# Kernel optimization log

Measured on AMD Instinct MI355X. Metric: run time of the kernel, lower is better.

Reference implementation:

```python
import jax, jax.numpy as jnp
import numpy as np

L, B, D, H, M, F = 384, 16, 1024, 16, 64, 4096
HD = D // H
LEFT, RIGHT = 64, 64
STD_SCALE = 0.5
LN_EPS = 1e-5


def layer_norm(x, w, b):
    mu = jnp.mean(x, axis=-1, keepdims=True)
    var = jnp.mean((x - mu) ** 2, axis=-1, keepdims=True)
    return (x - mu) / jnp.sqrt(var + LN_EPS) * w + b


def linear(x, w, b):  # torch nn.Linear: y = x @ W^T + b, w is [out, in]
    return x @ w.T + b


def attention_suppression(aw, scale):
    # aw: [N, Tq, Tk] raw logits (may contain -inf)
    p = jax.nn.softmax(aw, axis=-1)
    nz = p > 0.0  # entries with -inf logits are exactly 0 after softmax
    nzs = jnp.sum(nz.astype(aw.dtype), axis=-1, keepdims=True)
    mean = jnp.sum(p, axis=-1, keepdims=True) / nzs
    dis = jnp.where(nz, (p - mean) ** 2, jnp.zeros_like(p))
    var = jnp.sum(dis, axis=-1, keepdims=True) / (nzs - 1.0)
    thr = mean - scale * jnp.sqrt(var)
    return jnp.where(p < thr, -jnp.inf, aw)


def setup_inputs() -> dict:
    key = jax.random.key(0)
    ks = jax.random.split(key, 24)
    s = 0.02

    def w(k, shape):
        return jax.random.normal(k, shape, dtype=jnp.float32) * s

    return {
        "x": jax.random.normal(ks[0], (L, B, D), dtype=jnp.float32),
        "memory": jax.random.normal(ks[1], (M, B, D), dtype=jnp.float32),
        "q_w": w(ks[2], (D, D)), "q_b": jnp.zeros((D,), jnp.float32),
        "k_w": w(ks[3], (D, D)), "k_b": jnp.zeros((D,), jnp.float32),
        "v_w": w(ks[4], (D, D)), "v_b": jnp.zeros((D,), jnp.float32),
        "out_w": w(ks[5], (D, D)), "out_b": jnp.zeros((D,), jnp.float32),
        "ln1_w": jnp.ones((D,), jnp.float32), "ln1_b": jnp.zeros((D,), jnp.float32),
        "fc1_w": w(ks[6], (F, D)), "fc1_b": jnp.zeros((F,), jnp.float32),
        "fc2_w": w(ks[7], (D, F)), "fc2_b": jnp.zeros((D,), jnp.float32),
        "ln2_w": jnp.ones((D,), jnp.float32), "ln2_b": jnp.zeros((D,), jnp.float32),
    }


def reference(x, memory, q_w, q_b, k_w, k_b, v_w, v_b, out_w, out_b,
              ln1_w, ln1_b, fc1_w, fc1_b, fc2_w, fc2_b, ln2_w, ln2_b):
    residual = x
    xn = layer_norm(x, ln1_w, ln1_b)  # normalize_before
    # summarization query = mean over segment (excluding left/right context)
    summary = jnp.mean(xn[LEFT:L - RIGHT], axis=0, keepdims=True)  # [1,B,D]
    inp = jnp.concatenate([xn, summary], axis=0)  # [L+1, B, D]
    mem_and_inp = jnp.concatenate([memory, inp[:-1]], axis=0)  # [M+L, B, D]

    scaling = HD ** -0.5
    q = linear(inp, q_w, q_b) * scaling
    k = linear(mem_and_inp, k_w, k_b)
    v = linear(mem_and_inp, v_w, v_b)

    def split_heads(t):  # [T,B,D] -> [B*H, T, HD]
        return t.reshape(t.shape[0], B * H, HD).transpose(1, 0, 2)

    q, k, v = split_heads(q), split_heads(k), split_heads(v)
    aw = jnp.einsum('nqd,nkd->nqk', q, k)  # [B*H, L+1, M+L]
    # disable mem-on-mem: summary (last) query must not attend to memory keys
    aw = aw.at[:, -1, :M].set(-jnp.inf)
    aw = attention_suppression(aw, STD_SCALE)
    p = jax.nn.softmax(aw, axis=-1)
    attn = jnp.einsum('nqk,nkd->nqd', p, v)  # [B*H, L+1, HD]
    attn = attn.transpose(1, 0, 2).reshape(L + 1, B, D)
    out_and_mem = linear(attn, out_w, out_b)
    # next_m = out_and_mem[-1:] appended to state (identity squash); output drops it
    out = out_and_mem[:-1]

    x = residual + out
    residual = x
    xn = layer_norm(x, ln2_w, ln2_b)
    h = jax.nn.relu(linear(xn, fc1_w, fc1_b))
    h = linear(h, fc2_w, fc2_b)
    return residual + h
```

## Files before the change

### kernel.cpp

```cpp
#include <hip/hip_runtime.h>

typedef __bf16 bf16x8 __attribute__((ext_vector_type(8)));
typedef float f32x4 __attribute__((ext_vector_type(4)));
typedef unsigned short u16x8 __attribute__((ext_vector_type(8)));

__device__ __forceinline__ unsigned short f2bf(float f) {
  union { float f; unsigned int u; } v; v.f = f;
  unsigned int r = v.u + 0x7fffu + ((v.u >> 16) & 1u);
  return (unsigned short)(r >> 16);
}

__device__ __forceinline__ void async16(const unsigned short* g, unsigned short* l) {
  __builtin_amdgcn_global_load_lds(
      (const __attribute__((address_space(1))) unsigned int*)g,
      (__attribute__((address_space(3))) unsigned int*)l, 16, 0, 0);
}

__global__ void cvt_all(const float* __restrict__ q_w, const float* __restrict__ k_w,
                        const float* __restrict__ v_w, const float* __restrict__ o_w,
                        const float* __restrict__ f1w, const float* __restrict__ f2w,
                        const float* __restrict__ mem,
                        const float* __restrict__ q_b, const float* __restrict__ k_b,
                        const float* __restrict__ v_b,
                        unsigned short* __restrict__ WQ, unsigned short* __restrict__ WK,
                        unsigned short* __restrict__ WV, unsigned short* __restrict__ WO,
                        unsigned short* __restrict__ WF1, unsigned short* __restrict__ WF2,
                        unsigned short* __restrict__ MEMB, float* __restrict__ QKVB) {
  const int bid = blockIdx.x;
  const float* src; unsigned short* dst; float scale = 1.f; int base;
  if (bid < 1024)       { src = q_w; dst = WQ;  scale = 0.125f; base = 0; }
  else if (bid < 2048)  { src = k_w; dst = WK;  base = 1024; }
  else if (bid < 3072)  { src = v_w; dst = WV;  base = 2048; }
  else if (bid < 4096)  { src = o_w; dst = WO;  base = 3072; }
  else if (bid < 8192)  { src = f1w; dst = WF1; base = 4096; }
  else if (bid < 12288) { src = f2w; dst = WF2; base = 8192; }
  else if (bid < 13312) { src = mem; dst = MEMB; base = 12288; }
  else {
    const int i = (bid - 13312) * 256 + threadIdx.x;
    QKVB[i] = (i < 1024) ? q_b[i] * 0.125f : (i < 2048 ? k_b[i - 1024] : v_b[i - 2048]);
    return;
  }
  const int i = (bid - base) * 256 + threadIdx.x;
  float4 v = ((const float4*)src)[i];
  ushort4 o;
  o.x = f2bf(v.x * scale); o.y = f2bf(v.y * scale);
  o.z = f2bf(v.z * scale); o.w = f2bf(v.w * scale);
  ((ushort4*)dst)[i] = o;
}

template <int PREFILL>
__global__ __launch_bounds__(256) void ln_bf16(
    const float* __restrict__ src, unsigned short* __restrict__ dst,
    const float* __restrict__ g, const float* __restrict__ be,
    const float* __restrict__ fbias, float* __restrict__ dout) {
  const int row = blockIdx.x, tid = threadIdx.x;
  const float4 v = ((const float4*)(src + (size_t)row * 1024))[tid];
  if (PREFILL) {
    const float4 fb = ((const float4*)fbias)[tid];
    float4 r;
    r.x = v.x + fb.x; r.y = v.y + fb.y; r.z = v.z + fb.z; r.w = v.w + fb.w;
    ((float4*)(dout + (size_t)row * 1024))[tid] = r;
  }
  float s = v.x + v.y + v.z + v.w;
  float qq = v.x * v.x + v.y * v.y + v.z * v.z + v.w * v.w;
#pragma unroll
  for (int off = 32; off; off >>= 1) { s += __shfl_xor(s, off); qq += __shfl_xor(qq, off); }
  __shared__ float ps[4], pq[4];
  const int w = tid >> 6, lane = tid & 63;
  if (lane == 0) { ps[w] = s; pq[w] = qq; }
  __syncthreads();
  if (tid == 0) { ps[0] = ps[0] + ps[1] + ps[2] + ps[3]; pq[0] = pq[0] + pq[1] + pq[2] + pq[3]; }
  __syncthreads();
  const float mu = ps[0] * (1.f / 1024.f);
  const float var = pq[0] * (1.f / 1024.f) - mu * mu;
  const float rs = rsqrtf(var + 1e-5f);
  const float4 gv = ((const float4*)g)[tid];
  const float4 bv = ((const float4*)be)[tid];
  ushort4 o;
  o.x = f2bf((v.x - mu) * rs * gv.x + bv.x);
  o.y = f2bf((v.y - mu) * rs * gv.y + bv.y);
  o.z = f2bf((v.z - mu) * rs * gv.z + bv.z);
  o.w = f2bf((v.w - mu) * rs * gv.w + bv.w);
  ((ushort4*)(dst + (size_t)row * 1024))[tid] = o;
}

#define KOFF 6291456ull
#define VOFF 13631488ull
template <int EPI>
__global__ __launch_bounds__(256) void gemm_bt(
    const unsigned short* __restrict__ A, const unsigned short* __restrict__ Bw,
    const float* __restrict__ bias, const float* __restrict__ resid,
    void* __restrict__ Cout, int M, int N, int K, int lda, int ldb, int NBN, int WM) {
  __shared__ __align__(16) unsigned short lA[128 * 32];
  __shared__ __align__(16) unsigned short lB[128 * 32];
  const int tid = threadIdx.x;
  const int w = tid >> 6, lane = tid & 63;
  const int lr = lane & 15, lq = lane >> 4;
  const int l = blockIdx.x;
  const int xcd = l & 7, r = l >> 3;
  const int bm = xcd * WM + (r % WM);
  const int rest = r / WM;
  const int bn = rest % NBN;
  const size_t koff = (size_t)(rest / NBN) * K;
  const unsigned short* Ab = A + (size_t)bm * 128 * lda + koff;
  const unsigned short* Bb = Bw + (size_t)bn * 128 * ldb + koff;
  const int wm = (w & 1) << 6, wn = (w >> 1) << 6;
  f32x4 acc[4][4] = {};
  const int kiters = K >> 5;
  const int c0 = tid, c1 = 256 + tid;
  const int r0 = c0 >> 2, o0 = (c0 & 3) << 3;
  const int r1 = c1 >> 2, o1 = (c1 & 3) << 3;
  for (int kt = 0; kt < kiters; ++kt) {
    const int kb = kt << 5;
    __syncthreads();
    async16(Ab + (size_t)r0 * lda + kb + o0, lA + c0 * 8);
    async16(Bb + (size_t)r0 * ldb + kb + o0, lB + c0 * 8);
    async16(Ab + (size_t)r1 * lda + kb + o1, lA + c1 * 8);
    async16(Bb + (size_t)r1 * ldb + kb + o1, lB + c1 * 8);
    __syncthreads();
    bf16x8 af[4], bfr[4];
#pragma unroll
    for (int i = 0; i < 4; ++i) af[i] = *(const bf16x8*)(lA + (wm + i * 16 + lr) * 32 + lq * 8);
#pragma unroll
    for (int i = 0; i < 4; ++i) bfr[i] = *(const bf16x8*)(lB + (wn + i * 16 + lr) * 32 + lq * 8);
#pragma unroll
    for (int i = 0; i < 4; ++i)
#pragma unroll
      for (int j = 0; j < 4; ++j)
        acc[i][j] = __builtin_amdgcn_mfma_f32_16x16x32_bf16(af[i], bfr[j], acc[i][j], 0, 0, 0);
  }
  const int which = (bn * 128) >> 10;
#pragma unroll
  for (int i = 0; i < 4; ++i) {
#pragma unroll
    for (int j = 0; j < 4; ++j) {
      const int colg = bn * 128 + wn + j * 16 + lr;
      const float bi = (EPI == 6) ? 0.f : bias[colg];
      const int rowg0 = bm * 128 + wm + i * 16 + lq * 4;
#pragma unroll
      for (int r2 = 0; r2 < 4; ++r2) {
        const int rowg = rowg0 + r2;
        const float val = acc[i][j][r2] + bi;
        if (EPI == 5) {
          const int t = rowg >> 4, bb = rowg & 15;
          const int hh = (colg >> 6) & 15, dd = colg & 63;
          const size_t nn = (size_t)(bb * 16 + hh);
          unsigned short* q16 = (unsigned short*)Cout;
          if (which == 0) {
            if (rowg >= 1024) q16[(nn * 384 + (t - 64)) * 64 + dd] = f2bf(val);
          } else if (which == 1) {
            q16[KOFF + (nn * 448 + t) * 64 + dd] = f2bf(val);
          } else {
            q16[VOFF + (nn * 448 + t) * 64 + dd] = f2bf(val);
          }
        } else {
          const size_t idx = (size_t)rowg * N + colg;
          if (EPI == 2) ((float*)Cout)[idx] = val + resid[idx];
          else if (EPI == 3) ((unsigned short*)Cout)[idx] = f2bf(fmaxf(val, 0.f));
          else if (EPI == 6) atomicAdd(&((float*)Cout)[idx], acc[i][j][r2]);
        }
      }
    }
  }
}

#define WAITV10() asm volatile("s_waitcnt vmcnt(10)" ::: "memory")
#define WAITV8()  asm volatile("s_waitcnt vmcnt(8)" ::: "memory")
#define WAITV0()  asm volatile("s_waitcnt vmcnt(0)" ::: "memory")
#define WAITL0()  asm volatile("s_waitcnt lgkmcnt(0)" ::: "memory")
#define BAR()     do { __builtin_amdgcn_s_barrier(); __builtin_amdgcn_sched_barrier(0); } while (0)
#define SCHED()   __builtin_amdgcn_sched_barrier(0)

#define STG_A(bufv, ksv, ktv) do { \
    unsigned short* d_ = (unsigned short*)lA8 + (bufv) * 16384 + (ksv) * 8192; \
    const unsigned short* s_ = Ab + (((ktv) << 6) + ((ksv) << 5)); \
    async16(s_ + (size_t)sr0 * lda + sc0, d_ + ci0 * 8); \
    async16(s_ + (size_t)sr1 * lda + sc1, d_ + ci1 * 8); } while (0)
#define STG_B(bufv, ksv, ktv) do { \
    unsigned short* d_ = (unsigned short*)lB8 + (bufv) * 16384 + (ksv) * 8192; \
    const unsigned short* s_ = Bb + (((ktv) << 6) + ((ksv) << 5)); \
    async16(s_ + (size_t)sr0 * ldb + sc0, d_ + ci0 * 8); \
    async16(s_ + (size_t)sr1 * ldb + sc1, d_ + ci1 * 8); } while (0)
#define RD_A4(dst, bufv, ksv, mh) \
  _Pragma("unroll") \
  for (int i = 0; i < 4; ++i) \
    dst[i] = *(const bf16x8*)((unsigned short*)lA8 + (bufv) * 16384 + (ksv) * 8192 + \
                              (wm * 128 + (mh) * 64 + i * 16 + lr) * 32 + lq * 8)
#define RD_B4(dst, bufv, ksv) \
  _Pragma("unroll") \
  for (int j = 0; j < 4; ++j) \
    dst[j] = *(const bf16x8*)((unsigned short*)lB8 + (bufv) * 16384 + (ksv) * 8192 + \
                              (wn * 64 + j * 16 + lr) * 32 + lq * 8)
#define MFMA16(accbase, av, bv) \
  _Pragma("unroll") \
  for (int i = 0; i < 4; ++i) \
  _Pragma("unroll") \
  for (int j = 0; j < 4; ++j) \
    acc[(accbase) + i][j] = \
        __builtin_amdgcn_mfma_f32_16x16x32_bf16(av[i], bv[j], acc[(accbase) + i][j], 0, 0, 0)

__global__ __launch_bounds__(512, 2) void gemm8_relu(
    const unsigned short* __restrict__ A, const unsigned short* __restrict__ Bw,
    const float* __restrict__ bias, unsigned short* __restrict__ Cout,
    int N, int lda, int ldb, int MT) {
  __shared__ __align__(16) unsigned short lA8[32768];
  __shared__ __align__(16) unsigned short lB8[32768];
  const int tid = threadIdx.x;
  const int w = tid >> 6, lane = tid & 63;
  const int wm = w >> 2, wn = w & 3;
  const int lr = lane & 15, lq = lane >> 4;
  const int bid = blockIdx.x;
  const int xcd = bid & 7, r = bid >> 3;
  const int bm = xcd * MT + (r % MT);
  const int bn = r / MT;
  const unsigned short* Ab = A + (size_t)bm * 256 * lda;
  const unsigned short* Bb = Bw + (size_t)bn * 256 * ldb;
  const int ci0 = tid, ci1 = tid + 512;
  const int sr0 = ci0 >> 2, sc0 = (ci0 & 3) << 3;
  const int sr1 = ci1 >> 2, sc1 = (ci1 & 3) << 3;

  f32x4 acc[8][4] = {};
  bf16x8 aP[4], aN[4], b0[4], b1[4];

  STG_B(0, 0, 0); STG_A(0, 0, 0); STG_B(0, 1, 0); STG_A(0, 1, 0);
  STG_B(1, 0, 1); STG_A(1, 0, 1); STG_B(1, 1, 1); STG_A(1, 1, 1);
  WAITV8();
  BAR();
  RD_A4(aP, 0, 0, 0);
  RD_B4(b0, 0, 0);

  for (int kt = 0; kt < 16; ++kt) {
    const int buf = kt & 1, nbuf = buf ^ 1, kt2 = kt + 2;
    const bool st = kt2 < 16, tail = kt >= 14;
    WAITL0(); if (tail) { WAITV0(); } else { WAITV10(); } BAR();
    if (st) STG_B(buf, 0, kt2);
    RD_A4(aN, buf, 0, 1);
    SCHED();
    __builtin_amdgcn_s_setprio(1);
    MFMA16(0, aP, b0);
    __builtin_amdgcn_s_setprio(0);
    WAITL0(); if (tail) { WAITV0(); } else { WAITV10(); } BAR();
    if (st) STG_A(buf, 0, kt2);
    RD_A4(aP, buf, 1, 0);
    RD_B4(b1, buf, 1);
    SCHED();
    __builtin_amdgcn_s_setprio(1);
    MFMA16(4, aN, b0);
    __builtin_amdgcn_s_setprio(0);
    WAITL0(); if (tail) { WAITV0(); } else { WAITV10(); } BAR();
    if (st) STG_B(buf, 1, kt2);
    RD_A4(aN, buf, 1, 1);
    SCHED();
    __builtin_amdgcn_s_setprio(1);
    MFMA16(0, aP, b1);
    __builtin_amdgcn_s_setprio(0);
    WAITL0(); if (tail) { WAITV0(); } else { WAITV10(); } BAR();
    if (st) STG_A(buf, 1, kt2);
    if (kt < 15) { RD_A4(aP, nbuf, 0, 0); RD_B4(b0, nbuf, 0); }
    SCHED();
    __builtin_amdgcn_s_setprio(1);
    MFMA16(4, aN, b1);
    __builtin_amdgcn_s_setprio(0);
  }

#pragma unroll
  for (int j = 0; j < 4; ++j) {
    const int colg = bn * 256 + wn * 64 + j * 16 + lr;
    const float bi = bias[colg];
#pragma unroll
    for (int i = 0; i < 8; ++i) {
      const int rowg0 = bm * 256 + wm * 128 + i * 16 + lq * 4;
#pragma unroll
      for (int r2 = 0; r2 < 4; ++r2) {
        const float v = acc[i][j][r2] + bi;
        Cout[(size_t)(rowg0 + r2) * N + colg] = f2bf(fmaxf(v, 0.f));
      }
    }
  }
}

__global__ __launch_bounds__(256) void vtrans(const unsigned short* __restrict__ vb,
                                              unsigned short* __restrict__ vt) {
  __shared__ __align__(16) unsigned short ls[64][80];
  const int kc = blockIdx.x, n = blockIdx.y;
  const int tid = threadIdx.x;
#pragma unroll
  for (int i = 0; i < 2; ++i) {
    const int c = i * 256 + tid;
    const int kk = c >> 3, dc = (c & 7) << 3;
    u16x8 val = *(const u16x8*)(vb + ((size_t)n * 448 + kc * 64 + kk) * 64 + dc);
    *(u16x8*)&ls[kk][dc] = val;
  }
  __syncthreads();
#pragma unroll
  for (int i = 0; i < 2; ++i) {
    const int c = i * 256 + tid;
    const int d = c >> 3, kx = (c & 7) << 3;
    u16x8 o;
#pragma unroll
    for (int j = 0; j < 8; ++j) o[j] = ls[kx + j][d];
    *(u16x8*)(vt + ((size_t)n * 64 + d) * 448 + kc * 64 + kx) = o;
  }
}

#define PST 468
__global__ __launch_bounds__(256) void attn_kernel(
    const unsigned short* __restrict__ qt_, const unsigned short* __restrict__ kt_,
    const unsigned short* __restrict__ vt_, unsigned short* __restrict__ attn) {
  __shared__ __align__(16) unsigned short P[16 * PST];
  __shared__ float Rm[4][16], Rs[4][16], Rc[4][16], Rv[4][16], R2[4][16];
  __shared__ __align__(16) float OT[4][16][17];
  const int id = blockIdx.x;
  const int xcd = id & 7, j0 = id >> 3;
  const int n = xcd * 32 + (j0 & 31), qt = j0 >> 5;
  const int b = n >> 4, h = n & 15;
  const int tid = threadIdx.x, w = tid >> 6, lane = tid & 63;
  const int lr = lane & 15, lq = lane >> 4;

  const unsigned short* qp = qt_ + ((size_t)n * 384 + qt * 16 + lr) * 64 + lq * 8;
  const bf16x8 q0 = *(const bf16x8*)qp;
  const bf16x8 q1 = *(const bf16x8*)(qp + 32);

  f32x4 acc[7];
#pragma unroll
  for (int t = 0; t < 7; ++t) {
    const unsigned short* kp = kt_ + ((size_t)n * 448 + (w * 7 + t) * 16 + lr) * 64 + lq * 8;
    const bf16x8 k0 = *(const bf16x8*)kp;
    const bf16x8 k1 = *(const bf16x8*)(kp + 32);
    f32x4 a = {0.f, 0.f, 0.f, 0.f};
    a = __builtin_amdgcn_mfma_f32_16x16x32_bf16(k0, q0, a, 0, 0, 0);
    a = __builtin_amdgcn_mfma_f32_16x16x32_bf16(k1, q1, a, 0, 0, 0);
    acc[t] = a;
  }

  f32x4 m4 = acc[0];
#pragma unroll
  for (int t = 1; t < 7; ++t) {
    m4[0] = fmaxf(m4[0], acc[t][0]); m4[1] = fmaxf(m4[1], acc[t][1]);
    m4[2] = fmaxf(m4[2], acc[t][2]); m4[3] = fmaxf(m4[3], acc[t][3]);
  }
  float m = fmaxf(fmaxf(m4[0], m4[1]), fmaxf(m4[2], m4[3]));
  m = fmaxf(m, __shfl_xor(m, 16));
  m = fmaxf(m, __shfl_xor(m, 32));
  if (lq == 0) Rm[w][lr] = m;
  __syncthreads();
  m = fmaxf(fmaxf(Rm[0][lr], Rm[1][lr]), fmaxf(Rm[2][lr], Rm[3][lr]));

  f32x4 s4 = {0.f, 0.f, 0.f, 0.f}, c4 = {0.f, 0.f, 0.f, 0.f};
#pragma unroll
  for (int t = 0; t < 7; ++t) {
#pragma unroll
    for (int r = 0; r < 4; ++r) {
      const float e = __expf(acc[t][r] - m);
      acc[t][r] = e;
      s4[r] += e;
      if (e > 0.f) c4[r] += 1.f;
    }
  }
  float s = (s4[0] + s4[1]) + (s4[2] + s4[3]);
  float cnt = (c4[0] + c4[1]) + (c4[2] + c4[3]);
  s += __shfl_xor(s, 16); s += __shfl_xor(s, 32);
  cnt += __shfl_xor(cnt, 16); cnt += __shfl_xor(cnt, 32);
  if (lq == 0) { Rs[w][lr] = s; Rc[w][lr] = cnt; }
  __syncthreads();
  s = (Rs[0][lr] + Rs[1][lr]) + (Rs[2][lr] + Rs[3][lr]);
  cnt = (Rc[0][lr] + Rc[1][lr]) + (Rc[2][lr] + Rc[3][lr]);
  const float inv = 1.f / s;
  const float mean = 1.f / cnt;

  f32x4 d4 = {0.f, 0.f, 0.f, 0.f};
#pragma unroll
  for (int t = 0; t < 7; ++t) {
#pragma unroll
    for (int r = 0; r < 4; ++r) {
      const float p = acc[t][r] * inv;
      const float dd = p - mean;
      if (acc[t][r] > 0.f) d4[r] += dd * dd;
    }
  }
  float dv = (d4[0] + d4[1]) + (d4[2] + d4[3]);
  dv += __shfl_xor(dv, 16); dv += __shfl_xor(dv, 32);
  if (lq == 0) Rv[w][lr] = dv;
  __syncthreads();
  dv = (Rv[0][lr] + Rv[1][lr]) + (Rv[2][lr] + Rv[3][lr]);
  const float thr = mean - 0.5f * sqrtf(dv / (cnt - 1.f));

  f32x4 t4 = {0.f, 0.f, 0.f, 0.f};
#pragma unroll
  for (int t = 0; t < 7; ++t) {
#pragma unroll
    for (int r = 0; r < 4; ++r) {
      if (!(acc[t][r] * inv < thr)) t4[r] += acc[t][r];
    }
  }
  float s2 = (t4[0] + t4[1]) + (t4[2] + t4[3]);
  s2 += __shfl_xor(s2, 16); s2 += __shfl_xor(s2, 32);
  if (lq == 0) R2[w][lr] = s2;
  __syncthreads();
  s2 = (R2[0][lr] + R2[1][lr]) + (R2[2][lr] + R2[3][lr]);
  const float inv2 = 1.f / s2;

#pragma unroll
  for (int t = 0; t < 7; ++t) {
#pragma unroll
    for (int rp = 0; rp < 4; rp += 2) {
      const float v0 = (acc[t][rp] * inv < thr) ? 0.f : acc[t][rp] * inv2;
      const float v1 = (acc[t][rp + 1] * inv < thr) ? 0.f : acc[t][rp + 1] * inv2;
      const unsigned int u = (unsigned int)f2bf(v0) | ((unsigned int)f2bf(v1) << 16);
      *(unsigned int*)&P[lr * PST + (w * 7 + t) * 16 + lq * 4 + rp] = u;
    }
  }
  __syncthreads();

  f32x4 o = {0.f, 0.f, 0.f, 0.f};
#pragma unroll
  for (int c = 0; c < 14; ++c) {
    union { ushort4 hh[2]; bf16x8 v; } bf;
    bf.hh[0] = *(const ushort4*)&P[lr * PST + c * 32 + lq * 8];
    bf.hh[1] = *(const ushort4*)&P[lr * PST + c * 32 + lq * 8 + 4];
    const bf16x8 a = *(const bf16x8*)(vt_ + ((size_t)n * 64 + w * 16 + lr) * 448 + c * 32 + lq * 8);
    o = __builtin_amdgcn_mfma_f32_16x16x32_bf16(a, bf.v, o, 0, 0, 0);
  }

#pragma unroll
  for (int r = 0; r < 4; ++r) OT[w][lq * 4 + r][lr] = o[r];
  const int qrow = lane >> 2, dg = lane & 3;
  ushort4 ov;
  ov.x = f2bf(OT[w][dg * 4 + 0][qrow]);
  ov.y = f2bf(OT[w][dg * 4 + 1][qrow]);
  ov.z = f2bf(OT[w][dg * 4 + 2][qrow]);
  ov.w = f2bf(OT[w][dg * 4 + 3][qrow]);
  *(ushort4*)(attn + ((size_t)(qt * 16 + qrow) * 16 + b) * 1024 + h * 64 + w * 16 + dg * 4) = ov;
}

extern "C" void kernel_launch(void* const* d_in, const int* in_sizes, int n_in,
                              void* d_out, int out_size, void* d_ws, size_t ws_size,
                              hipStream_t stream) {
  (void)in_sizes; (void)n_in; (void)out_size; (void)ws_size;
  const float* x    = (const float*)d_in[0];
  const float* mem  = (const float*)d_in[1];
  const float* q_w  = (const float*)d_in[2];
  const float* q_b  = (const float*)d_in[3];
  const float* k_w  = (const float*)d_in[4];
  const float* k_b  = (const float*)d_in[5];
  const float* v_w  = (const float*)d_in[6];
  const float* v_b  = (const float*)d_in[7];
  const float* o_w  = (const float*)d_in[8];
  const float* o_b  = (const float*)d_in[9];
  const float* ln1w = (const float*)d_in[10];
  const float* ln1b = (const float*)d_in[11];
  const float* f1w  = (const float*)d_in[12];
  const float* f1b  = (const float*)d_in[13];
  const float* f2w  = (const float*)d_in[14];
  const float* f2b  = (const float*)d_in[15];
  const float* ln2w = (const float*)d_in[16];
  const float* ln2b = (const float*)d_in[17];

  unsigned short* WQ   = (unsigned short*)d_ws;
  unsigned short* WK   = WQ + 1048576;
  unsigned short* WV   = WK + 1048576;
  unsigned short* WO   = WV + 1048576;
  unsigned short* WF1  = WO + 1048576;
  unsigned short* WF2  = WF1 + 4194304;
  unsigned short* ABUF = WF2 + 4194304;
  unsigned short* QB   = ABUF + 7340032;
  unsigned short* KB   = QB + 6291456;
  unsigned short* VB   = KB + 7340032;
  unsigned short* VT   = VB + 7340032;
  unsigned short* ATTN = VT + 7340032;
  float*          X2   = (float*)(ATTN + 6291456);
  float*          QKVB = (float*)ATTN;
  unsigned short* XN2  = ATTN;
  unsigned short* HB   = ABUF;

  cvt_all<<<13324, 256, 0, stream>>>(q_w, k_w, v_w, o_w, f1w, f2w, mem, q_b, k_b, v_b,
                                     WQ, WK, WV, WO, WF1, WF2, ABUF, QKVB);

  ln_bf16<0><<<6144, 256, 0, stream>>>(x, ABUF + 1048576, ln1w, ln1b, nullptr, nullptr);

  gemm_bt<5><<<1344, 256, 0, stream>>>(ABUF, WQ, QKVB, nullptr, QB, 7168, 3072, 1024, 1024, 1024, 24, 7);

  vtrans<<<dim3(7, 256), 256, 0, stream>>>(VB, VT);
  attn_kernel<<<6144, 256, 0, stream>>>(QB, KB, VT, ATTN);

  gemm_bt<2><<<384, 256, 0, stream>>>(ATTN, WO, o_b, x, X2, 6144, 1024, 1024, 1024, 1024, 8, 6);

  ln_bf16<1><<<6144, 256, 0, stream>>>(X2, XN2, ln2w, ln2b, f2b, (float*)d_out);

  gemm8_relu<<<384, 512, 0, stream>>>(XN2, WF1, f1b, HB, 4096, 1024, 1024, 3);
  gemm_bt<6><<<768, 256, 0, stream>>>(HB, WF2, nullptr, nullptr, d_out, 6144, 1024, 2048, 4096, 4096, 8, 6);
}
```

Measured before the change: 548.2 us.

## Shrink FC1 GEMM tile to 256x128 and double grid; add occupancy hint to gemm_bt

```diff
diff --git a/kernel.cpp b/kernel.cpp
--- a/kernel.cpp
+++ b/kernel.cpp
@@ -87,7 +87,7 @@
 #define KOFF 6291456ull
 #define VOFF 13631488ull
 template <int EPI>
-__global__ __launch_bounds__(256) void gemm_bt(
+__global__ __launch_bounds__(256, 8) void gemm_bt(
     const unsigned short* __restrict__ A, const unsigned short* __restrict__ Bw,
     const float* __restrict__ bias, const float* __restrict__ resid,
     void* __restrict__ Cout, int M, int N, int K, int lda, int ldb, int NBN, int WM) {
@@ -164,8 +164,7 @@
   }
 }
 
-#define WAITV10() asm volatile("s_waitcnt vmcnt(10)" ::: "memory")
-#define WAITV8()  asm volatile("s_waitcnt vmcnt(8)" ::: "memory")
+#define WAITV6()  asm volatile("s_waitcnt vmcnt(6)" ::: "memory")
 #define WAITV0()  asm volatile("s_waitcnt vmcnt(0)" ::: "memory")
 #define WAITL0()  asm volatile("s_waitcnt lgkmcnt(0)" ::: "memory")
 #define BAR()     do { __builtin_amdgcn_s_barrier(); __builtin_amdgcn_sched_barrier(0); } while (0)
@@ -174,102 +173,88 @@
 #define STG_A(bufv, ksv, ktv) do { \
     unsigned short* d_ = (unsigned short*)lA8 + (bufv) * 16384 + (ksv) * 8192; \
     const unsigned short* s_ = Ab + (((ktv) << 6) + ((ksv) << 5)); \
-    async16(s_ + (size_t)sr0 * lda + sc0, d_ + ci0 * 8); \
-    async16(s_ + (size_t)sr1 * lda + sc1, d_ + ci1 * 8); } while (0)
+    async16(s_ + (size_t)ar0 * lda + ac0, d_ + ci0 * 8); \
+    async16(s_ + (size_t)ar1 * lda + ac1, d_ + ci1 * 8); } while (0)
 #define STG_B(bufv, ksv, ktv) do { \
-    unsigned short* d_ = (unsigned short*)lB8 + (bufv) * 16384 + (ksv) * 8192; \
+    unsigned short* d_ = (unsigned short*)lB8 + (bufv) * 8192 + (ksv) * 4096; \
     const unsigned short* s_ = Bb + (((ktv) << 6) + ((ksv) << 5)); \
-    async16(s_ + (size_t)sr0 * ldb + sc0, d_ + ci0 * 8); \
-    async16(s_ + (size_t)sr1 * ldb + sc1, d_ + ci1 * 8); } while (0)
-#define RD_A4(dst, bufv, ksv, mh) \
+    async16(s_ + (size_t)br0 * ldb + bc0, d_ + tid * 8); } while (0)
+#define RD_A4(dst, bufv, ksv) \
   _Pragma("unroll") \
   for (int i = 0; i < 4; ++i) \
     dst[i] = *(const bf16x8*)((unsigned short*)lA8 + (bufv) * 16384 + (ksv) * 8192 + \
-                              (wm * 128 + (mh) * 64 + i * 16 + lr) * 32 + lq * 8)
+                              (wm * 64 + i * 16 + lr) * 32 + lq * 8)
 #define RD_B4(dst, bufv, ksv) \
   _Pragma("unroll") \
   for (int j = 0; j < 4; ++j) \
-    dst[j] = *(const bf16x8*)((unsigned short*)lB8 + (bufv) * 16384 + (ksv) * 8192 + \
+    dst[j] = *(const bf16x8*)((unsigned short*)lB8 + (bufv) * 8192 + (ksv) * 4096 + \
                               (wn * 64 + j * 16 + lr) * 32 + lq * 8)
-#define MFMA16(accbase, av, bv) \
+#define MFMA16(av, bv) \
   _Pragma("unroll") \
   for (int i = 0; i < 4; ++i) \
   _Pragma("unroll") \
   for (int j = 0; j < 4; ++j) \
-    acc[(accbase) + i][j] = \
-        __builtin_amdgcn_mfma_f32_16x16x32_bf16(av[i], bv[j], acc[(accbase) + i][j], 0, 0, 0)
+    acc[i][j] = \
+        __builtin_amdgcn_mfma_f32_16x16x32_bf16(av[i], bv[j], acc[i][j], 0, 0, 0)
 
 __global__ __launch_bounds__(512, 2) void gemm8_relu(
     const unsigned short* __restrict__ A, const unsigned short* __restrict__ Bw,
     const float* __restrict__ bias, unsigned short* __restrict__ Cout,
     int N, int lda, int ldb, int MT) {
   __shared__ __align__(16) unsigned short lA8[32768];
-  __shared__ __align__(16) unsigned short lB8[32768];
+  __shared__ __align__(16) unsigned short lB8[16384];
   const int tid = threadIdx.x;
   const int w = tid >> 6, lane = tid & 63;
-  const int wm = w >> 2, wn = w & 3;
+  const int wm = w >> 1, wn = w & 1;
   const int lr = lane & 15, lq = lane >> 4;
   const int bid = blockIdx.x;
   const int xcd = bid & 7, r = bid >> 3;
   const int bm = xcd * MT + (r % MT);
   const int bn = r / MT;
   const unsigned short* Ab = A + (size_t)bm * 256 * lda;
-  const unsigned short* Bb = Bw + (size_t)bn * 256 * ldb;
+  const unsigned short* Bb = Bw + (size_t)bn * 128 * ldb;
   const int ci0 = tid, ci1 = tid + 512;
-  const int sr0 = ci0 >> 2, sc0 = (ci0 & 3) << 3;
-  const int sr1 = ci1 >> 2, sc1 = (ci1 & 3) << 3;
-
-  f32x4 acc[8][4] = {};
+  const int ar0 = ci0 >> 2, ac0 = (ci0 & 3) << 3;
+  const int ar1 = ci1 >> 2, ac1 = (ci1 & 3) << 3;
+  const int br0 = tid >> 2, bc0 = (tid & 3) << 3;
+
+  f32x4 acc[4][4] = {};
   bf16x8 aP[4], aN[4], b0[4], b1[4];
 
   STG_B(0, 0, 0); STG_A(0, 0, 0); STG_B(0, 1, 0); STG_A(0, 1, 0);
   STG_B(1, 0, 1); STG_A(1, 0, 1); STG_B(1, 1, 1); STG_A(1, 1, 1);
-  WAITV8();
+  WAITV6();
   BAR();
-  RD_A4(aP, 0, 0, 0);
+  RD_A4(aP, 0, 0);
   RD_B4(b0, 0, 0);
 
   for (int kt = 0; kt < 16; ++kt) {
     const int buf = kt & 1, nbuf = buf ^ 1, kt2 = kt + 2;
     const bool st = kt2 < 16, tail = kt >= 14;
-    WAITL0(); if (tail) { WAITV0(); } else { WAITV10(); } BAR();
-    if (st) STG_B(buf, 0, kt2);
-    RD_A4(aN, buf, 0, 1);
-    SCHED();
-    __builtin_amdgcn_s_setprio(1);
-    MFMA16(0, aP, b0);
-    __builtin_amdgcn_s_setprio(0);
-    WAITL0(); if (tail) { WAITV0(); } else { WAITV10(); } BAR();
-    if (st) STG_A(buf, 0, kt2);
-    RD_A4(aP, buf, 1, 0);
+    WAITL0(); if (tail) { WAITV0(); } else { WAITV6(); } BAR();
+    if (st) { STG_B(buf, 0, kt2); STG_A(buf, 0, kt2); }
+    RD_A4(aN, buf, 1);
     RD_B4(b1, buf, 1);
     SCHED();
     __builtin_amdgcn_s_setprio(1);
-    MFMA16(4, aN, b0);
+    MFMA16(aP, b0);
     __builtin_amdgcn_s_setprio(0);
-    WAITL0(); if (tail) { WAITV0(); } else { WAITV10(); } BAR();
-    if (st) STG_B(buf, 1, kt2);
-    RD_A4(aN, buf, 1, 1);
+    WAITL0(); if (tail) { WAITV0(); } else { WAITV6(); } BAR();
+    if (st) { STG_B(buf, 1, kt2); STG_A(buf, 1, kt2); }
+    if (kt < 15) { RD_A4(aP, nbuf, 0); RD_B4(b0, nbuf, 0); }
     SCHED();
     __builtin_amdgcn_s_setprio(1);
-    MFMA16(0, aP, b1);
+    MFMA16(aN, b1);
     __builtin_amdgcn_s_setprio(0);
-    WAITL0(); if (tail) { WAITV0(); } else { WAITV10(); } BAR();
-    if (st) STG_A(buf, 1, kt2);
-    if (kt < 15) { RD_A4(aP, nbuf, 0, 0); RD_B4(b0, nbuf, 0); }
-    SCHED();
-    __builtin_amdgcn_s_setprio(1);
-    MFMA16(4, aN, b1);
-    __builtin_amdgcn_s_setprio(0);
   }
 
 #pragma unroll
   for (int j = 0; j < 4; ++j) {
-    const int colg = bn * 256 + wn * 64 + j * 16 + lr;
+    const int colg = bn * 128 + wn * 64 + j * 16 + lr;
     const float bi = bias[colg];
 #pragma unroll
-    for (int i = 0; i < 8; ++i) {
-      const int rowg0 = bm * 256 + wm * 128 + i * 16 + lq * 4;
+    for (int i = 0; i < 4; ++i) {
+      const int rowg0 = bm * 256 + wm * 64 + i * 16 + lq * 4;
 #pragma unroll
       for (int r2 = 0; r2 < 4; ++r2) {
         const float v = acc[i][j][r2] + bi;
@@ -487,6 +472,6 @@
 
   ln_bf16<1><<<6144, 256, 0, stream>>>(X2, XN2, ln2w, ln2b, f2b, (float*)d_out);
 
-  gemm8_relu<<<384, 512, 0, stream>>>(XN2, WF1, f1b, HB, 4096, 1024, 1024, 3);
+  gemm8_relu<<<768, 512, 0, stream>>>(XN2, WF1, f1b, HB, 4096, 1024, 1024, 3);
   gemm_bt<6><<<768, 256, 0, stream>>>(HB, WF2, nullptr, nullptr, d_out, 6144, 1024, 2048, 4096, 4096, 8, 6);
 }
```

Result: slower. 1.647 ms (+200.4%).
